# Kernel optimization log

Measured on AMD Instinct MI355X. Metric: run time of the kernel, lower is better.

## Reference

```python
import jax, jax.numpy as jnp
import numpy as np

B, T, D, K = 4, 4096, 1024, 64


def setup_inputs() -> dict:
    key = jax.random.key(0)
    k1, k2, k3, k4 = jax.random.split(key, 4)
    x = jax.random.normal(k1, (B, T, D), dtype=jnp.float32)
    Wq = jax.random.normal(k2, (D, K), dtype=jnp.float32) * (D ** -0.5)
    Wk = jax.random.normal(k3, (D, K), dtype=jnp.float32) * (D ** -0.5)
    Wv = jax.random.normal(k4, (D, D), dtype=jnp.float32) * (D ** -0.5)
    return {"x": x, "Wq": Wq, "Wk": Wk, "Wv": Wv}


def reference(x, Wq, Wk, Wv):
    # x: (B,T,D); single-head causal self-attention with value dim = D
    Bx, Tx, Dx = x.shape
    head_size = Wq.shape[-1]
    q = jnp.einsum('btd,dk->btk', x, Wq)  # (B,T,K)
    k = jnp.einsum('btd,dk->btk', x, Wk)  # (B,T,K)
    v = jnp.einsum('btd,de->bte', x, Wv)  # (B,T,D)
    scores = jnp.einsum('bqk,bsk->bqs', q, k) * (head_size ** -0.5)  # (B,T,T)
    causal = jnp.tril(jnp.ones((Tx, Tx), dtype=bool))
    scores = jnp.where(causal[None, :, :], scores, -jnp.inf)
    attn = jax.nn.softmax(scores, axis=-1)
    return jnp.einsum('bqs,bsd->bqd', attn, v)  # (B,T,D)
```

## Files before the change

### kernel.cpp

```cpp
#include <hip/hip_runtime.h>
#include <hip/hip_bf16.h>

typedef __attribute__((ext_vector_type(8))) short bf16x8;
typedef __attribute__((ext_vector_type(4))) float f32x4;
typedef unsigned short u16;

#define MFMA16(a, b, c) __builtin_amdgcn_mfma_f32_16x16x32_bf16((a), (b), (c), 0, 0, 0)
#define GLLDS(gp, lp)                                                                  \
  __builtin_amdgcn_global_load_lds((const __attribute__((address_space(1))) unsigned int*)(gp), \
                                   (__attribute__((address_space(3))) unsigned int*)(lp), 16, 0, 0)

__device__ __forceinline__ u16 f2b(float f) {
  union { float f; unsigned u; } x; x.f = f;
  return (u16)((x.u + 0x7FFFu + ((x.u >> 16) & 1u)) >> 16);
}
__device__ __forceinline__ u16 f2b_hw(float f) {
  union { __hip_bfloat16 h; u16 u; } c;
  c.h = __float2bfloat16(f);
  return c.u;
}

__global__ __launch_bounds__(256) void k_cvt(const float* __restrict__ in,
                                             u16* __restrict__ out, int n4) {
  int i = blockIdx.x * 256 + threadIdx.x;
  if (i >= n4) return;
  float4 v = ((const float4*)in)[i];
  u16 a = f2b(v.x), b = f2b(v.y), c = f2b(v.z), d = f2b(v.w);
  ((uint2*)out)[i] = make_uint2((unsigned)a | ((unsigned)b << 16),
                                (unsigned)c | ((unsigned)d << 16));
}

__global__ __launch_bounds__(256) void k_packT(const float* __restrict__ in,
                                               u16* __restrict__ out, int R, int C) {
  __shared__ float t[32][33];
  int r0 = blockIdx.x * 32, c0 = blockIdx.y * 32;
  int cx = threadIdx.x & 31, ry = threadIdx.x >> 5;
#pragma unroll
  for (int k = 0; k < 4; k++)
    t[ry + k * 8][cx] = in[(size_t)(r0 + ry + k * 8) * C + c0 + cx];
  __syncthreads();
#pragma unroll
  for (int k = 0; k < 4; k++)
    out[(size_t)(c0 + ry + k * 8) * R + r0 + cx] = f2b(t[cx][ry + k * 8]);
}

__global__ __launch_bounds__(256) void k_gemm_qk(const u16* __restrict__ xb,
                                                 const u16* __restrict__ wqt,
                                                 const u16* __restrict__ wkt,
                                                 u16* __restrict__ q, u16* __restrict__ kk) {
  int row0 = blockIdx.x * 64;
  int tid = threadIdx.x, w = tid >> 6, l = tid & 63, l15 = l & 15, lg = l >> 4;
  const u16* wt = (w < 2) ? wqt : wkt;
  int nbase = (w & 1) * 32;
  f32x4 acc[4][2];
#pragma unroll
  for (int mt = 0; mt < 4; mt++)
#pragma unroll
    for (int nt = 0; nt < 2; nt++) acc[mt][nt] = (f32x4){0.f, 0.f, 0.f, 0.f};

  for (int k0 = 0; k0 < 1024; k0 += 32) {
    bf16x8 bfr[2], afr[4];
#pragma unroll
    for (int nt = 0; nt < 2; nt++)
      bfr[nt] = *(const bf16x8*)&wt[(size_t)(nbase + nt * 16 + l15) * 1024 + k0 + lg * 8];
#pragma unroll
    for (int mt = 0; mt < 4; mt++)
      afr[mt] = *(const bf16x8*)&xb[(size_t)(row0 + mt * 16 + l15) * 1024 + k0 + lg * 8];
#pragma unroll
    for (int mt = 0; mt < 4; mt++)
#pragma unroll
      for (int nt = 0; nt < 2; nt++) acc[mt][nt] = MFMA16(afr[mt], bfr[nt], acc[mt][nt]);
  }
  if (w < 2) {
#pragma unroll
    for (int mt = 0; mt < 4; mt++)
#pragma unroll
      for (int nt = 0; nt < 2; nt++)
#pragma unroll
        for (int j = 0; j < 4; j++)
          q[(size_t)(row0 + mt * 16 + lg * 4 + j) * 64 + nbase + nt * 16 + l15] =
              f2b(acc[mt][nt][j] * 0.125f);
  } else {
#pragma unroll
    for (int mt = 0; mt < 4; mt++)
#pragma unroll
      for (int nt = 0; nt < 2; nt++)
#pragma unroll
        for (int j = 0; j < 4; j++) {
          int row = row0 + mt * 16 + lg * 4 + j;
          int c = (nbase + nt * 16 + l15) * 2;
          size_t off = (size_t)(row >> 6) * 8192 + (row & 63) * 128 + (c ^ ((row & 7) << 4));
          *(u16*)((char*)kk + off) = f2b(acc[mt][nt][j]);
        }
  }
}

__global__ __launch_bounds__(256) void k_gemm_v(const u16* __restrict__ xb,
                                                const u16* __restrict__ wvt,
                                                u16* __restrict__ vT) {
  int b = blockIdx.z;
  int d0 = blockIdx.y * 128;
  int s0 = blockIdx.x * 128;
  int tid = threadIdx.x, w = tid >> 6, l = tid & 63, l15 = l & 15, lg = l >> 4;
  int wd = (w & 1) * 64, wsn = (w >> 1) * 64;
  __shared__ __align__(16) char lds[32768];

  const u16* arow = wvt + (size_t)d0 * 1024;
  const u16* brow = xb + (size_t)(b * 4096 + s0) * 1024;

  auto stage = [&](int buf, int k0) {
    char* La = lds + buf * 16384;
    char* Lb = La + 8192;
#pragma unroll
    for (int i = 0; i < 2; i++) {
      int row = w * 32 + i * 16 + (l >> 2), kq = (l & 3) * 8;
      GLLDS(&arow[(size_t)row * 1024 + k0 + kq], La + (w * 2 + i) * 1024);
      GLLDS(&brow[(size_t)row * 1024 + k0 + kq], Lb + (w * 2 + i) * 1024);
    }
  };

  f32x4 acc[4][4];
#pragma unroll
  for (int mt = 0; mt < 4; mt++)
#pragma unroll
    for (int nt = 0; nt < 4; nt++) acc[mt][nt] = (f32x4){0.f, 0.f, 0.f, 0.f};

  stage(0, 0);
  __syncthreads();
  int buf = 0;
  for (int k = 0; k < 32; k++) {
    if (k < 31) stage(buf ^ 1, (k + 1) * 32);
    const char* La = lds + buf * 16384;
    const char* Lb = La + 8192;
    bf16x8 afr[4], bfr[4];
#pragma unroll
    for (int mt = 0; mt < 4; mt++)
      afr[mt] = *(const bf16x8*)(La + (wd + mt * 16 + l15) * 64 + lg * 16);
#pragma unroll
    for (int nt = 0; nt < 4; nt++)
      bfr[nt] = *(const bf16x8*)(Lb + (wsn + nt * 16 + l15) * 64 + lg * 16);
    __builtin_amdgcn_s_setprio(1);
#pragma unroll
    for (int mt = 0; mt < 4; mt++)
#pragma unroll
      for (int nt = 0; nt < 4; nt++) acc[mt][nt] = MFMA16(afr[mt], bfr[nt], acc[mt][nt]);
    __builtin_amdgcn_s_setprio(0);
    __syncthreads();
    buf ^= 1;
  }
#pragma unroll
  for (int mt = 0; mt < 4; mt++)
#pragma unroll
    for (int nt = 0; nt < 4; nt++)
#pragma unroll
      for (int j = 0; j < 4; j++) {
        int d = d0 + wd + mt * 16 + lg * 4 + j;
        int s = s0 + wsn + nt * 16 + l15;
        size_t off = ((size_t)(b * 64 + (s >> 6)) * 8 + (d >> 7)) * 16384 + (d & 127) * 128 +
                     (((s & 63) * 2) ^ ((d & 7) << 4));
        *(u16*)((char*)vT + off) = f2b(acc[mt][nt][j]);
      }
}

__global__ __launch_bounds__(512, 2) void k_attn(const u16* __restrict__ qw,
                                                 const u16* __restrict__ kws,
                                                 const u16* __restrict__ vts,
                                                 float* __restrict__ out) {
  int bid = blockIdx.x;
  int xcd = bid & 7, rest = bid >> 3;
  int p = rest & 15, hi = rest >> 4;
  int g = xcd + 8 * hi;
  int cpair = g & 3, b = g >> 2;
  int tid = threadIdx.x, w = tid >> 6, l = tid & 63, l15 = l & 15, lg = l >> 4;
  int sw = (l15 & 7) << 4;
  size_t tokb = (size_t)b * 4096;

  __shared__ __align__(16) char lds[66048];
  char* Pb = lds + 49152;
  float* scb = (float*)(lds + 65536);

  const short ob = (short)0x3F80;
  const bf16x8 ones = {ob, ob, ob, ob, ob, ob, ob, ob};
  const bf16x8 zf = {0, 0, 0, 0, 0, 0, 0, 0};

  auto stageV = [&](int t) {
    const char* vb = (const char*)vts + ((size_t)(b * 64 + t) * 8 + cpair * 2) * 16384;
    char* lv = lds + 16384;
#pragma unroll
    for (int i = 0; i < 4; i++) {
      int s = w * 4 + i;
      GLLDS(vb + s * 1024 + l * 16, lv + s * 1024);
    }
  };
  auto stageK = [&](int t, int bufi) {
    const char* kb = (const char*)kws + (size_t)(b * 64 + t) * 8192;
    GLLDS(kb + w * 1024 + l * 16, lds + bufi * 8192 + w * 1024);
  };

  auto run_phase = [&](int Q0) {
    int ntb = (Q0 >> 6) + 2;
    int qsA = Q0 + w * 16;
    int qA = qsA + l15;
    int qsB = Q0 + (w & 3) * 32;
    int dhalf = w >> 2;

    bf16x8 qf[2];
#pragma unroll
    for (int ks = 0; ks < 2; ks++)
      qf[ks] = *(const bf16x8*)&qw[(tokb + qA) * 64 + ks * 32 + lg * 8];

    f32x4 acc[8][2], accl[2];
    float mrow = -1e30f;
#pragma unroll
    for (int mt = 0; mt < 8; mt++)
#pragma unroll
      for (int qt = 0; qt < 2; qt++) acc[mt][qt] = (f32x4){0.f, 0.f, 0.f, 0.f};
    accl[0] = (f32x4){0.f, 0.f, 0.f, 0.f};
    accl[1] = (f32x4){0.f, 0.f, 0.f, 0.f};

    stageK(0, 0);
    __syncthreads();
    int buf = 0;
    for (int t = 0; t < ntb; t++) {
      int s0 = t * 64;
      stageV(t);
      if (t + 1 < ntb) stageK(t + 1, buf ^ 1);
      if (s0 < qsA + 16) {
        const char* Kb = lds + buf * 8192;
        f32x4 sfr[4];
        __builtin_amdgcn_s_setprio(1);
#pragma unroll
        for (int nt = 0; nt < 4; nt++) {
          const char* kr = Kb + (nt * 16 + l15) * 128;
          bf16x8 kf0 = *(const bf16x8*)(kr + ((lg * 16) ^ sw));
          bf16x8 kf1 = *(const bf16x8*)(kr + ((64 + lg * 16) ^ sw));
          f32x4 z = (f32x4){0.f, 0.f, 0.f, 0.f};
          z = MFMA16(kf0, qf[0], z);
          sfr[nt] = MFMA16(kf1, qf[1], z);
        }
        __builtin_amdgcn_s_setprio(0);
        if (s0 + 63 > qsA) {
#pragma unroll
          for (int nt = 0; nt < 4; nt++)
#pragma unroll
            for (int j = 0; j < 4; j++)
              if (s0 + nt * 16 + lg * 4 + j > qA) sfr[nt][j] = -1e30f;
        }
        float pm = fmaxf(fmaxf(fmaxf(sfr[0][0], sfr[0][1]), fmaxf(sfr[0][2], sfr[0][3])),
                         fmaxf(fmaxf(sfr[1][0], sfr[1][1]), fmaxf(sfr[1][2], sfr[1][3])));
        pm = fmaxf(pm, fmaxf(fmaxf(fmaxf(sfr[2][0], sfr[2][1]), fmaxf(sfr[2][2], sfr[2][3])),
                             fmaxf(fmaxf(sfr[3][0], sfr[3][1]), fmaxf(sfr[3][2], sfr[3][3]))));
        pm = fmaxf(pm, __shfl_xor(pm, 16));
        pm = fmaxf(pm, __shfl_xor(pm, 32));
        float sc = 1.0f;
        if (__any(pm > mrow + 8.0f)) {
          float mn = fmaxf(mrow, pm);
          sc = __expf(mrow - mn);
          mrow = mn;
        }
        int rq = w * 16 + l15;
        scb[rq] = sc;
        int rbase = rq * 128, sx = (rq & 7) << 4;
#pragma unroll
        for (int nt = 0; nt < 4; nt++) {
          unsigned lo = (unsigned)f2b_hw(__expf(sfr[nt][0] - mrow)) |
                        ((unsigned)f2b_hw(__expf(sfr[nt][1] - mrow)) << 16);
          unsigned hi2 = (unsigned)f2b_hw(__expf(sfr[nt][2] - mrow)) |
                         ((unsigned)f2b_hw(__expf(sfr[nt][3] - mrow)) << 16);
          int addr = (rbase + (nt * 16 + lg * 4) * 2) ^ sx;
          *(uint2*)(Pb + addr) = make_uint2(lo, hi2);
        }
      }
      __syncthreads();
      if (s0 < qsB + 32) {
        const char* Vb = lds + 16384 + dhalf * 16384;
        bool act0 = s0 < qsB + 16;
        int R0 = (w & 3) * 32 + l15;
        if (act0) {
          float sq0 = scb[R0];
          if (!__all(sq0 == 1.0f)) {
#pragma unroll
            for (int mt = 0; mt < 8; mt++) acc[mt][0] *= sq0;
            accl[0] *= sq0;
          }
        }
        {
          float sq1 = scb[R0 + 16];
          if (!__all(sq1 == 1.0f)) {
#pragma unroll
            for (int mt = 0; mt < 8; mt++) acc[mt][1] *= sq1;
            accl[1] *= sq1;
          }
        }
        bf16x8 pf00 = zf, pf01 = zf, pf10, pf11;
        if (act0) {
          int rx = (R0 & 7) << 4;
          pf00 = *(const bf16x8*)(Pb + ((R0 * 128 + lg * 16) ^ rx));
          pf01 = *(const bf16x8*)(Pb + ((R0 * 128 + 64 + lg * 16) ^ rx));
        }
        {
          int R1 = R0 + 16, rx = (R1 & 7) << 4;
          pf10 = *(const bf16x8*)(Pb + ((R1 * 128 + lg * 16) ^ rx));
          pf11 = *(const bf16x8*)(Pb + ((R1 * 128 + 64 + lg * 16) ^ rx));
        }
        __builtin_amdgcn_s_setprio(1);
        accl[0] = MFMA16(ones, pf00, accl[0]);
        accl[0] = MFMA16(ones, pf01, accl[0]);
        accl[1] = MFMA16(ones, pf10, accl[1]);
        accl[1] = MFMA16(ones, pf11, accl[1]);
#pragma unroll
        for (int mt = 0; mt < 8; mt++) {
          const char* vr = Vb + (mt * 16 + l15) * 128;
          bf16x8 va0 = *(const bf16x8*)(vr + ((lg * 16) ^ sw));
          bf16x8 va1 = *(const bf16x8*)(vr + ((64 + lg * 16) ^ sw));
          acc[mt][0] = MFMA16(va0, pf00, acc[mt][0]);
          acc[mt][0] = MFMA16(va1, pf01, acc[mt][0]);
          acc[mt][1] = MFMA16(va0, pf10, acc[mt][1]);
          acc[mt][1] = MFMA16(va1, pf11, acc[mt][1]);
        }
        __builtin_amdgcn_s_setprio(0);
      }
      __syncthreads();
      buf ^= 1;
    }
#pragma unroll
    for (int qt = 0; qt < 2; qt++) {
      float linv = 1.0f / accl[qt][0];
#pragma unroll
      for (int mt = 0; mt < 8; mt++) {
        f32x4 v = acc[mt][qt] * linv;
        size_t o = (tokb + qsB + qt * 16 + l15) * 1024 + cpair * 256 + dhalf * 128 +
                   mt * 16 + lg * 4;
        *(f32x4*)&out[o] = v;
      }
    }
  };

  run_phase(p * 128);
  run_phase((31 - p) * 128);
}

extern "C" void kernel_launch(void* const* d_in, const int* in_sizes, int n_in,
                              void* d_out, int out_size, void* d_ws, size_t ws_size,
                              hipStream_t stream) {
  const float* x  = (const float*)d_in[0];
  const float* Wq = (const float*)d_in[1];
  const float* Wk = (const float*)d_in[2];
  const float* Wv = (const float*)d_in[3];
  float* out = (float*)d_out;
  char* ws = (char*)d_ws;
  u16* xb  = (u16*)(ws);
  u16* qw  = (u16*)(ws + 33554432);
  u16* kw  = (u16*)(ws + 35651584);
  u16* vT  = (u16*)(ws + 37748736);
  u16* wqt = (u16*)(ws + 71303168);
  u16* wkt = (u16*)(ws + 71434240);
  u16* wvt = (u16*)(ws + 71565312);

  k_cvt<<<16384, 256, 0, stream>>>(x, xb, 4194304);
  k_packT<<<dim3(32, 2), 256, 0, stream>>>(Wq, wqt, 1024, 64);
  k_packT<<<dim3(32, 2), 256, 0, stream>>>(Wk, wkt, 1024, 64);
  k_packT<<<dim3(32, 32), 256, 0, stream>>>(Wv, wvt, 1024, 1024);
  k_gemm_qk<<<256, 256, 0, stream>>>(xb, wqt, wkt, qw, kw);
  k_gemm_v<<<dim3(32, 8, 4), 256, 0, stream>>>(xb, wvt, vT);
  k_attn<<<256, 512, 0, stream>>>(qw, kw, vT, out);
}
```

Baseline: 219.3 us.

## Software-pipeline attention: compute next tile's scores while accumulating current PV

Restructures the attention loop so the QK^T/softmax stage for tile t+1 runs in the same barrier interval as the PV accumulation for tile t. V, P and the scale buffers become double-buffered, and K is prefetched two tiles ahead. This removes one __syncthreads per iteration and lets score MFMAs and exp work overlap with PV MFMAs. The cost is LDS use growing from about 66KB to 113KB per block, which may reduce occupancy below the two blocks per CU requested in launch bounds.

Result: no change. 218.2 us (-0.5%).

```diff
diff --git a/kernel.cpp b/kernel.cpp
--- a/kernel.cpp
+++ b/kernel.cpp
@@ -175,22 +175,17 @@
   int sw = (l15 & 7) << 4;
   size_t tokb = (size_t)b * 4096;
 
-  __shared__ __align__(16) char lds[66048];
-  char* Pb = lds + 49152;
-  float* scb = (float*)(lds + 65536);
+  __shared__ __align__(16) char lds[115712];
 
   const short ob = (short)0x3F80;
   const bf16x8 ones = {ob, ob, ob, ob, ob, ob, ob, ob};
   const bf16x8 zf = {0, 0, 0, 0, 0, 0, 0, 0};
 
-  auto stageV = [&](int t) {
+  auto stageV = [&](int t, int bufi) {
     const char* vb = (const char*)vts + ((size_t)(b * 64 + t) * 8 + cpair * 2) * 16384;
-    char* lv = lds + 16384;
-#pragma unroll
-    for (int i = 0; i < 4; i++) {
-      int s = w * 4 + i;
-      GLLDS(vb + s * 1024 + l * 16, lv + s * 1024);
-    }
+    char* lv = lds + 16384 + bufi * 32768;
+#pragma unroll
+    for (int i = 0; i < 4; i++) GLLDS(vb + (w * 4 + i) * 1024 + l * 16, lv + (w * 4 + i) * 1024);
   };
   auto stageK = [&](int t, int bufi) {
     const char* kb = (const char*)kws + (size_t)(b * 64 + t) * 8192;
@@ -218,62 +213,75 @@
     accl[0] = (f32x4){0.f, 0.f, 0.f, 0.f};
     accl[1] = (f32x4){0.f, 0.f, 0.f, 0.f};
 
+    auto doA = [&](int ta) {
+      int s0 = ta * 64;
+      if (s0 >= qsA + 16) return;
+      int bi = ta & 1;
+      const char* Kb = lds + bi * 8192;
+      char* Pw = lds + 81920 + bi * 16384;
+      float* scw = (float*)(lds + 114688) + bi * 128;
+      f32x4 sfr[4];
+      __builtin_amdgcn_s_setprio(1);
+#pragma unroll
+      for (int nt = 0; nt < 4; nt++) {
+        const char* kr = Kb + (nt * 16 + l15) * 128;
+        bf16x8 kf0 = *(const bf16x8*)(kr + ((lg * 16) ^ sw));
+        bf16x8 kf1 = *(const bf16x8*)(kr + ((64 + lg * 16) ^ sw));
+        f32x4 z = (f32x4){0.f, 0.f, 0.f, 0.f};
+        z = MFMA16(kf0, qf[0], z);
+        sfr[nt] = MFMA16(kf1, qf[1], z);
+      }
+      __builtin_amdgcn_s_setprio(0);
+      if (s0 + 63 > qsA) {
+#pragma unroll
+        for (int nt = 0; nt < 4; nt++)
+#pragma unroll
+          for (int j = 0; j < 4; j++)
+            if (s0 + nt * 16 + lg * 4 + j > qA) sfr[nt][j] = -1e30f;
+      }
+      float pm = fmaxf(fmaxf(fmaxf(sfr[0][0], sfr[0][1]), fmaxf(sfr[0][2], sfr[0][3])),
+                       fmaxf(fmaxf(sfr[1][0], sfr[1][1]), fmaxf(sfr[1][2], sfr[1][3])));
+      pm = fmaxf(pm, fmaxf(fmaxf(fmaxf(sfr[2][0], sfr[2][1]), fmaxf(sfr[2][2], sfr[2][3])),
+                           fmaxf(fmaxf(sfr[3][0], sfr[3][1]), fmaxf(sfr[3][2], sfr[3][3]))));
+      pm = fmaxf(pm, __shfl_xor(pm, 16));
+      pm = fmaxf(pm, __shfl_xor(pm, 32));
+      float sc = 1.0f;
+      if (__any(pm > mrow + 8.0f)) {
+        float mn = fmaxf(mrow, pm);
+        sc = __expf(mrow - mn);
+        mrow = mn;
+      }
+      int rq = w * 16 + l15;
+      scw[rq] = sc;
+      int rbase = rq * 128, sx = (rq & 7) << 4;
+#pragma unroll
+      for (int nt = 0; nt < 4; nt++) {
+        unsigned lo = (unsigned)f2b_hw(__expf(sfr[nt][0] - mrow)) |
+                      ((unsigned)f2b_hw(__expf(sfr[nt][1] - mrow)) << 16);
+        unsigned hi2 = (unsigned)f2b_hw(__expf(sfr[nt][2] - mrow)) |
+                       ((unsigned)f2b_hw(__expf(sfr[nt][3] - mrow)) << 16);
+        int addr = (rbase + (nt * 16 + lg * 4) * 2) ^ sx;
+        *(uint2*)(Pw + addr) = make_uint2(lo, hi2);
+      }
+    };
+
     stageK(0, 0);
+    stageV(0, 0);
     __syncthreads();
-    int buf = 0;
+    doA(0);
+    stageK(1, 1);
+    __syncthreads();
+
     for (int t = 0; t < ntb; t++) {
+      if (t + 1 < ntb) stageV(t + 1, (t + 1) & 1);
+      if (t + 2 < ntb) stageK(t + 2, t & 1);
+      doA(t + 1);
       int s0 = t * 64;
-      stageV(t);
-      if (t + 1 < ntb) stageK(t + 1, buf ^ 1);
-      if (s0 < qsA + 16) {
-        const char* Kb = lds + buf * 8192;
-        f32x4 sfr[4];
-        __builtin_amdgcn_s_setprio(1);
-#pragma unroll
-        for (int nt = 0; nt < 4; nt++) {
-          const char* kr = Kb + (nt * 16 + l15) * 128;
-          bf16x8 kf0 = *(const bf16x8*)(kr + ((lg * 16) ^ sw));
-          bf16x8 kf1 = *(const bf16x8*)(kr + ((64 + lg * 16) ^ sw));
-          f32x4 z = (f32x4){0.f, 0.f, 0.f, 0.f};
-          z = MFMA16(kf0, qf[0], z);
-          sfr[nt] = MFMA16(kf1, qf[1], z);
-        }
-        __builtin_amdgcn_s_setprio(0);
-        if (s0 + 63 > qsA) {
-#pragma unroll
-          for (int nt = 0; nt < 4; nt++)
-#pragma unroll
-            for (int j = 0; j < 4; j++)
-              if (s0 + nt * 16 + lg * 4 + j > qA) sfr[nt][j] = -1e30f;
-        }
-        float pm = fmaxf(fmaxf(fmaxf(sfr[0][0], sfr[0][1]), fmaxf(sfr[0][2], sfr[0][3])),
-                         fmaxf(fmaxf(sfr[1][0], sfr[1][1]), fmaxf(sfr[1][2], sfr[1][3])));
-        pm = fmaxf(pm, fmaxf(fmaxf(fmaxf(sfr[2][0], sfr[2][1]), fmaxf(sfr[2][2], sfr[2][3])),
-                             fmaxf(fmaxf(sfr[3][0], sfr[3][1]), fmaxf(sfr[3][2], sfr[3][3]))));
-        pm = fmaxf(pm, __shfl_xor(pm, 16));
-        pm = fmaxf(pm, __shfl_xor(pm, 32));
-        float sc = 1.0f;
-        if (__any(pm > mrow + 8.0f)) {
-          float mn = fmaxf(mrow, pm);
-          sc = __expf(mrow - mn);
-          mrow = mn;
-        }
-        int rq = w * 16 + l15;
-        scb[rq] = sc;
-        int rbase = rq * 128, sx = (rq & 7) << 4;
-#pragma unroll
-        for (int nt = 0; nt < 4; nt++) {
-          unsigned lo = (unsigned)f2b_hw(__expf(sfr[nt][0] - mrow)) |
-                        ((unsigned)f2b_hw(__expf(sfr[nt][1] - mrow)) << 16);
-          unsigned hi2 = (unsigned)f2b_hw(__expf(sfr[nt][2] - mrow)) |
-                         ((unsigned)f2b_hw(__expf(sfr[nt][3] - mrow)) << 16);
-          int addr = (rbase + (nt * 16 + lg * 4) * 2) ^ sx;
-          *(uint2*)(Pb + addr) = make_uint2(lo, hi2);
-        }
-      }
-      __syncthreads();
       if (s0 < qsB + 32) {
-        const char* Vb = lds + 16384 + dhalf * 16384;
+        int bi = t & 1;
+        const char* Pb = lds + 81920 + bi * 16384;
+        const float* scb = (const float*)(lds + 114688) + bi * 128;
+        const char* Vb = lds + 16384 + bi * 32768 + dhalf * 16384;
         bool act0 = s0 < qsB + 16;
         int R0 = (w & 3) * 32 + l15;
         if (act0) {
@@ -321,7 +329,6 @@
         __builtin_amdgcn_s_setprio(0);
       }
       __syncthreads();
-      buf ^= 1;
     }
 #pragma unroll
     for (int qt = 0; qt < 2; qt++) {
```
